# Optimization experiments

Measured on AMD Instinct MI355X. Metric: run time of the kernel, lower is better.

## Reference

```python
import jax, jax.numpy as jnp
import numpy as np

# The 8 structuring elements from the torch module, in order.
_KERNELS = np.array([
    [[1.,1.,1.],[1.,1.,1.],[1.,1.,1.]],
    [[0.,1.,1.],[0.,1.,1.],[0.,1.,1.]],
    [[1.,1.,1.],[1.,1.,1.],[0.,0.,0.]],
    [[0.,0.,0.],[0.,1.,1.],[0.,1.,1.]],
    [[0.,1.,0.],[0.,1.,0.],[0.,1.,0.]],
    [[0.,0.,0.],[1.,1.,1.],[0.,0.,0.]],
    [[0.,1.,0.],[0.,1.,0.],[0.,0.,0.]],
    [[0.,0.,0.],[1.,1.,0.],[0.,0.,0.]],
], dtype=np.float32)


def _conv3x3(x, k):
    # x: [N,1,H,W], k: [3,3] -> same-padded single-channel conv (cross-correlation, like torch conv2d)
    return jax.lax.conv_general_dilated(
        x, k[None, None, :, :], window_strides=(1, 1),
        padding=((1, 1), (1, 1)),
        dimension_numbers=('NCHW', 'OIHW', 'NCHW'))


def setup_inputs() -> dict:
    key = jax.random.key(0)
    N, H, W = 16, 1024, 1024
    x = (jax.random.uniform(key, (N, 1, H, W)) < 0.5).astype(jnp.float32)
    kernels = jnp.asarray(_KERNELS)  # [8,3,3]
    return {"x": x, "kernels": kernels}


def reference(x, kernels):
    output = jnp.zeros_like(x)
    # Sequential loop over the 8 fixed structuring elements (data dependency on x).
    for i in range(8):
        k = kernels[i]
        eroded = _conv3x3(x, k)
        ksum = jnp.sum(k)
        mask = (eroded >= ksum).astype(x.dtype)
        output = jnp.maximum(output, mask)
        # mark(): dilate the mask with the flipped binarized kernel
        dil_k = jnp.flip((k > 0).astype(x.dtype), axis=(0, 1))
        visited = (_conv3x3(mask, dil_k) > 0).astype(x.dtype)
        x = x - visited
    # return_single_point=True branch
    sp = _conv3x3(output, kernels[0])
    output = jnp.where((sp > 0) & (sp < 2), jnp.ones_like(sp), jnp.zeros_like(sp))
    return output
```

## Files before the change

kernel.cpp:

```cpp
#include <hip/hip_runtime.h>
#include <stdint.h>


typedef unsigned long long u64;

#define WIDTH   1024
#define HEIGHT  1024
#define NIMG    16
#define WPR     16
#define TH      64
#define TWW     4
#define RROWS   96
#define RWORDS  6
#define PR      98
#define PW      8

__global__ __launch_bounds__(256) void pack_kernel(const float* __restrict__ x,
                                                   u64* __restrict__ packed) {
    int rowg = blockIdx.x;
    int tid  = threadIdx.x;
    int wv   = tid >> 6;
    int lane = tid & 63;
    const float* base = x + (size_t)rowg * WIDTH + wv * 256;
    u64* pbase = packed + (size_t)rowg * WPR + wv * 4;
    #pragma unroll
    for (int j = 0; j < 4; ++j) {
        float f = base[j * 64 + lane];
        u64 m = __ballot(f > 0.5f);
        if (lane == 0) pbase[j] = m;
    }
}

__device__ __forceinline__ u64 hrow_and(const u64* Ar, int w, int rowbits) {
    u64 res = ~0ULL;
    u64 c = Ar[w];
    if (rowbits & 1) res &= (c << 1) | (Ar[w - 1] >> 63);
    if (rowbits & 2) res &= c;
    if (rowbits & 4) res &= (c >> 1) | (Ar[w + 1] << 63);
    return res;
}
__device__ __forceinline__ u64 hrow_or(const u64* Ar, int w, int rowbits) {
    u64 res = 0;
    u64 c = Ar[w];
    if (rowbits & 1) res |= (c >> 1) | (Ar[w + 1] << 63);
    if (rowbits & 2) res |= c;
    if (rowbits & 4) res |= (c << 1) | (Ar[w - 1] >> 63);
    return res;
}

template <int KM>
__device__ __forceinline__ u64 erode_cell(const u64 (*A)[PW], int r, int w) {
    u64 res = ~0ULL;
    if ((KM >> 0) & 7) res &= hrow_and(A[r - 1], w, (KM >> 0) & 7);
    if ((KM >> 3) & 7) res &= hrow_and(A[r    ], w, (KM >> 3) & 7);
    if ((KM >> 6) & 7) res &= hrow_and(A[r + 1], w, (KM >> 6) & 7);
    return res;
}
template <int KM>
__device__ __forceinline__ u64 dilate_cell(const u64 (*A)[PW], int r, int w) {
    u64 res = 0;
    if ((KM >> 0) & 7) res |= hrow_or(A[r + 1], w, (KM >> 0) & 7);
    if ((KM >> 3) & 7) res |= hrow_or(A[r    ], w, (KM >> 3) & 7);
    if ((KM >> 6) & 7) res |= hrow_or(A[r - 1], w, (KM >> 6) & 7);
    return res;
}

template <int KM>
__device__ __forceinline__ void morph_step(u64 (&B)[PR][PW], u64 (&M)[PR][PW],
                                           u64 (&O)[PR][PW], int tid) {
    for (int cell = tid; cell < RROWS * RWORDS; cell += 256) {
        int r = 1 + cell / RWORDS;
        int w = 1 + cell % RWORDS;
        u64 m = erode_cell<KM>(B, r, w);
        M[r][w] = m;
        O[r][w] |= m;
    }
    __syncthreads();
    for (int cell = tid; cell < RROWS * RWORDS; cell += 256) {
        int r = 1 + cell / RWORDS;
        int w = 1 + cell % RWORDS;
        B[r][w] &= ~dilate_cell<KM>(M, r, w);
    }
    __syncthreads();
}

__global__ __launch_bounds__(256) void morph_kernel(const u64* __restrict__ packed,
                                                    float* __restrict__ out) {
    __shared__ u64 B[PR][PW];
    __shared__ u64 M[PR][PW];
    __shared__ u64 O[PR][PW];
    int tid = threadIdx.x;
    int tx = blockIdx.x, ty = blockIdx.y, img = blockIdx.z;

    {
        u64* bf = &B[0][0]; u64* mf = &M[0][0]; u64* of = &O[0][0];
        for (int i = tid; i < PR * PW; i += 256) { bf[i] = 0; mf[i] = 0; of[i] = 0; }
    }
    __syncthreads();

    const u64* pimg = packed + (size_t)img * HEIGHT * WPR;
    for (int cell = tid; cell < RROWS * RWORDS; cell += 256) {
        int r = cell / RWORDS, w = cell % RWORDS;
        int gy = ty * TH - 16 + r;
        int gw = tx * TWW - 1 + w;
        if (gy >= 0 && gy < HEIGHT && gw >= 0 && gw < WPR)
            B[r + 1][w + 1] = pimg[(size_t)gy * WPR + gw];
    }
    __syncthreads();

    morph_step<511>(B, M, O, tid);
    morph_step<438>(B, M, O, tid);
    morph_step< 63>(B, M, O, tid);
    morph_step<432>(B, M, O, tid);
    morph_step<146>(B, M, O, tid);
    morph_step< 56>(B, M, O, tid);
    morph_step< 18>(B, M, O, tid);
    morph_step< 24>(B, M, O, tid);

    {
        int w = 2 + (tid & 3);
        int r = 17 + (tid >> 2);
        u64 ones = 0, twos = 0;
        #pragma unroll
        for (int dr = -1; dr <= 1; ++dr) {
            const u64* Ar = O[r + dr];
            u64 c  = Ar[w];
            u64 wv = (c << 1) | (Ar[w - 1] >> 63);
            u64 ev = (c >> 1) | (Ar[w + 1] << 63);
            twos |= ones & wv; ones ^= wv;
            twos |= ones & c;  ones ^= c;
            twos |= ones & ev; ones ^= ev;
        }
        M[r][w] = ones & ~twos;
    }
    __syncthreads();

    float* obase = out + ((size_t)img * HEIGHT + (size_t)ty * TH) * WIDTH + tx * (TWW * 64);
    int w = 2 + (tid >> 6);
    int bit = tid & 63;
    for (int row = 0; row < TH; ++row) {
        u64 word = M[17 + row][w];
        obase[(size_t)row * WIDTH + tid] = (float)((word >> bit) & 1ULL);
    }
}

extern "C" void kernel_launch(void* const* d_in, const int* in_sizes, int n_in,
                              void* d_out, int out_size, void* d_ws, size_t ws_size,
                              hipStream_t stream) {
    const float* x = (const float*)d_in[0];
    float* out = (float*)d_out;
    u64* packed = (u64*)d_ws;

    hipLaunchKernelGGL(pack_kernel, dim3(NIMG * HEIGHT), dim3(256), 0, stream, x, packed);
    hipLaunchKernelGGL(morph_kernel,
                       dim3(WIDTH / (TWW * 64), HEIGHT / TH, NIMG), dim3(256), 0, stream,
                       packed, out);
}
```

Baseline: 136.7 us.

## Use full-width row tiles with separable erosion and shrinking halo regions

Each morph block now covers the full image width (16 words) instead of 4-word column tiles, which removes the redundant horizontal halo loads and work. Each rectangular kernel is split into a horizontal then a vertical pass through a temp buffer, and each step only processes the halo rows still needed, which cuts the cell count as the steps proceed. Blocks grow to 512 threads and the output is written with float4 stores. The cost is more barriers per step and fewer blocks (256 in total), which may leave the GPU underoccupied.

After: 125.9 us. 7.9% less time.

```diff
diff --git a/kernel.cpp b/kernel.cpp
--- a/kernel.cpp
+++ b/kernel.cpp
@@ -9,11 +9,9 @@
 #define NIMG    16
 #define WPR     16
 #define TH      64
-#define TWW     4
-#define RROWS   96
-#define RWORDS  6
 #define PR      98
-#define PW      8
+#define PW      18
+#define NTHR    512
 
 __global__ __launch_bounds__(256) void pack_kernel(const float* __restrict__ x,
                                                    u64* __restrict__ packed) {
@@ -31,96 +29,114 @@
     }
 }
 
-__device__ __forceinline__ u64 hrow_and(const u64* Ar, int w, int rowbits) {
-    u64 res = ~0ULL;
-    u64 c = Ar[w];
-    if (rowbits & 1) res &= (c << 1) | (Ar[w - 1] >> 63);
-    if (rowbits & 2) res &= c;
-    if (rowbits & 4) res &= (c >> 1) | (Ar[w + 1] << 63);
+template <int CM>
+__device__ __forceinline__ u64 hand(const u64* Ar, int w) {
+    u64 c = Ar[w], res = ~0ULL;
+    if (CM & 2) res &= c;
+    if (CM & 1) res &= (c << 1) | (Ar[w - 1] >> 63);
+    if (CM & 4) res &= (c >> 1) | (Ar[w + 1] << 63);
     return res;
 }
-__device__ __forceinline__ u64 hrow_or(const u64* Ar, int w, int rowbits) {
+template <int CM>
+__device__ __forceinline__ u64 hor(const u64* Ar, int w) {
+    u64 c = Ar[w], res = 0;
+    if (CM & 2) res |= c;
+    if (CM & 1) res |= (c >> 1) | (Ar[w + 1] << 63);
+    if (CM & 4) res |= (c << 1) | (Ar[w - 1] >> 63);
+    return res;
+}
+template <int RM>
+__device__ __forceinline__ u64 vand(const u64 (*A)[PW], int r, int w) {
+    u64 res = ~0ULL;
+    if (RM & 1) res &= A[r - 1][w];
+    if (RM & 2) res &= A[r][w];
+    if (RM & 4) res &= A[r + 1][w];
+    return res;
+}
+template <int RM>
+__device__ __forceinline__ u64 vor(const u64 (*A)[PW], int r, int w) {
     u64 res = 0;
-    u64 c = Ar[w];
-    if (rowbits & 1) res |= (c >> 1) | (Ar[w + 1] << 63);
-    if (rowbits & 2) res |= c;
-    if (rowbits & 4) res |= (c << 1) | (Ar[w - 1] >> 63);
+    if (RM & 1) res |= A[r + 1][w];
+    if (RM & 2) res |= A[r][w];
+    if (RM & 4) res |= A[r - 1][w];
     return res;
 }
 
-template <int KM>
-__device__ __forceinline__ u64 erode_cell(const u64 (*A)[PW], int r, int w) {
-    u64 res = ~0ULL;
-    if ((KM >> 0) & 7) res &= hrow_and(A[r - 1], w, (KM >> 0) & 7);
-    if ((KM >> 3) & 7) res &= hrow_and(A[r    ], w, (KM >> 3) & 7);
-    if ((KM >> 6) & 7) res &= hrow_and(A[r + 1], w, (KM >> 6) & 7);
-    return res;
-}
-template <int KM>
-__device__ __forceinline__ u64 dilate_cell(const u64 (*A)[PW], int r, int w) {
-    u64 res = 0;
-    if ((KM >> 0) & 7) res |= hrow_or(A[r + 1], w, (KM >> 0) & 7);
-    if ((KM >> 3) & 7) res |= hrow_or(A[r    ], w, (KM >> 3) & 7);
-    if ((KM >> 6) & 7) res |= hrow_or(A[r - 1], w, (KM >> 6) & 7);
-    return res;
-}
-
-template <int KM>
-__device__ __forceinline__ void morph_step(u64 (&B)[PR][PW], u64 (&M)[PR][PW],
-                                           u64 (&O)[PR][PW], int tid) {
-    for (int cell = tid; cell < RROWS * RWORDS; cell += 256) {
-        int r = 1 + cell / RWORDS;
-        int w = 1 + cell % RWORDS;
-        u64 m = erode_cell<KM>(B, r, w);
-        M[r][w] = m;
-        O[r][w] |= m;
-    }
-    __syncthreads();
-    for (int cell = tid; cell < RROWS * RWORDS; cell += 256) {
-        int r = 1 + cell / RWORDS;
-        int w = 1 + cell % RWORDS;
-        B[r][w] &= ~dilate_cell<KM>(M, r, w);
+template <int R, typename F>
+__device__ __forceinline__ void forcells(F f) {
+    for (int idx = threadIdx.x; idx < (TH + 2 * R) * WPR; idx += NTHR) {
+        int r = 17 - R + (idx >> 4);
+        int w = 1 + (idx & 15);
+        f(r, w);
     }
     __syncthreads();
 }
 
-__global__ __launch_bounds__(256) void morph_kernel(const u64* __restrict__ packed,
-                                                    float* __restrict__ out) {
+template <int RM, int CM, int HR, int MR, int DHR, int BR, bool DIL>
+__device__ __forceinline__ void morph_step(u64 (&B)[PR][PW], u64 (&T)[PR][PW],
+                                           u64 (&M)[PR][PW], u64 (&O)[PR][PW]) {
+    if (CM != 2 && RM != 2) {
+        forcells<HR>([&](int r, int w) { T[r][w] = hand<CM>(B[r], w); });
+        forcells<MR>([&](int r, int w) {
+            u64 m = vand<RM>(T, r, w); M[r][w] = m; O[r][w] |= m;
+        });
+    } else if (CM == 2) {
+        forcells<MR>([&](int r, int w) {
+            u64 m = vand<RM>(B, r, w); M[r][w] = m; O[r][w] |= m;
+        });
+    } else {
+        forcells<MR>([&](int r, int w) {
+            u64 m = hand<CM>(B[r], w); M[r][w] = m; O[r][w] |= m;
+        });
+    }
+    if (DIL) {
+        if (CM != 2 && RM != 2) {
+            forcells<DHR>([&](int r, int w) { T[r][w] = hor<CM>(M[r], w); });
+            forcells<BR>([&](int r, int w) { B[r][w] &= ~vor<RM>(T, r, w); });
+        } else if (CM == 2) {
+            forcells<BR>([&](int r, int w) { B[r][w] &= ~vor<RM>(M, r, w); });
+        } else {
+            forcells<BR>([&](int r, int w) { B[r][w] &= ~hor<CM>(M[r], w); });
+        }
+    }
+}
+
+__global__ __launch_bounds__(NTHR) void morph_kernel(const u64* __restrict__ packed,
+                                                     float* __restrict__ out) {
     __shared__ u64 B[PR][PW];
+    __shared__ u64 T[PR][PW];
     __shared__ u64 M[PR][PW];
     __shared__ u64 O[PR][PW];
     int tid = threadIdx.x;
-    int tx = blockIdx.x, ty = blockIdx.y, img = blockIdx.z;
+    int ty = blockIdx.x, img = blockIdx.y;
 
     {
         u64* bf = &B[0][0]; u64* mf = &M[0][0]; u64* of = &O[0][0];
-        for (int i = tid; i < PR * PW; i += 256) { bf[i] = 0; mf[i] = 0; of[i] = 0; }
+        for (int i = tid; i < PR * PW; i += NTHR) { bf[i] = 0; mf[i] = 0; of[i] = 0; }
     }
     __syncthreads();
 
     const u64* pimg = packed + (size_t)img * HEIGHT * WPR;
-    for (int cell = tid; cell < RROWS * RWORDS; cell += 256) {
-        int r = cell / RWORDS, w = cell % RWORDS;
-        int gy = ty * TH - 16 + r;
-        int gw = tx * TWW - 1 + w;
-        if (gy >= 0 && gy < HEIGHT && gw >= 0 && gw < WPR)
-            B[r + 1][w + 1] = pimg[(size_t)gy * WPR + gw];
+    for (int idx = tid; idx < (TH + 32) * WPR; idx += NTHR) {
+        int rr = idx >> 4, w = idx & 15;
+        int gy = ty * TH - 16 + rr;
+        if (gy >= 0 && gy < HEIGHT)
+            B[rr + 1][w + 1] = pimg[(size_t)gy * WPR + w];
     }
     __syncthreads();
 
-    morph_step<511>(B, M, O, tid);
-    morph_step<438>(B, M, O, tid);
-    morph_step< 63>(B, M, O, tid);
-    morph_step<432>(B, M, O, tid);
-    morph_step<146>(B, M, O, tid);
-    morph_step< 56>(B, M, O, tid);
-    morph_step< 18>(B, M, O, tid);
-    morph_step< 24>(B, M, O, tid);
+    morph_step<7, 7, 16, 15, 15, 14, true >(B, T, M, O);
+    morph_step<7, 6, 14, 13, 13, 12, true >(B, T, M, O);
+    morph_step<3, 7, 12, 11, 11, 10, true >(B, T, M, O);
+    morph_step<6, 6, 10,  9,  9,  8, true >(B, T, M, O);
+    morph_step<7, 2,  8,  7,  7,  6, true >(B, T, M, O);
+    morph_step<2, 7,  6,  5,  5,  4, true >(B, T, M, O);
+    morph_step<3, 2,  4,  3,  3,  2, true >(B, T, M, O);
+    morph_step<2, 3,  2,  1,  1,  0, false>(B, T, M, O);
 
-    {
-        int w = 2 + (tid & 3);
-        int r = 17 + (tid >> 2);
-        u64 ones = 0, twos = 0;
+    forcells<0>([&](int r, int w) {
+        u64 ones = 0;
+        u64 twos = 0;
         #pragma unroll
         for (int dr = -1; dr <= 1; ++dr) {
             const u64* Ar = O[r + dr];
@@ -131,16 +147,21 @@
             twos |= ones & c;  ones ^= c;
             twos |= ones & ev; ones ^= ev;
         }
-        M[r][w] = ones & ~twos;
-    }
-    __syncthreads();
+        T[r][w] = ones & ~twos;
+    });
 
-    float* obase = out + ((size_t)img * HEIGHT + (size_t)ty * TH) * WIDTH + tx * (TWW * 64);
-    int w = 2 + (tid >> 6);
-    int bit = tid & 63;
-    for (int row = 0; row < TH; ++row) {
-        u64 word = M[17 + row][w];
-        obase[(size_t)row * WIDTH + tid] = (float)((word >> bit) & 1ULL);
+    float* obase = out + ((size_t)img * HEIGHT + (size_t)ty * TH) * WIDTH;
+    for (int idx = tid; idx < TH * (WIDTH / 4); idx += NTHR) {
+        int row = idx >> 8;
+        int q   = idx & 255;
+        u64 word = T[17 + row][1 + (q >> 4)];
+        int b = (q & 15) * 4;
+        float4 v;
+        v.x = (float)((word >> (b + 0)) & 1ULL);
+        v.y = (float)((word >> (b + 1)) & 1ULL);
+        v.z = (float)((word >> (b + 2)) & 1ULL);
+        v.w = (float)((word >> (b + 3)) & 1ULL);
+        *(float4*)(obase + (size_t)row * WIDTH + q * 4) = v;
     }
 }
 
@@ -152,7 +173,6 @@
     u64* packed = (u64*)d_ws;
 
     hipLaunchKernelGGL(pack_kernel, dim3(NIMG * HEIGHT), dim3(256), 0, stream, x, packed);
-    hipLaunchKernelGGL(morph_kernel,
-                       dim3(WIDTH / (TWW * 64), HEIGHT / TH, NIMG), dim3(256), 0, stream,
+    hipLaunchKernelGGL(morph_kernel, dim3(HEIGHT / TH, NIMG), dim3(NTHR), 0, stream,
                        packed, out);
 }
```
